# Performance work log

Hardware: AMD Instinct MI355X
Metric: run time of the kernel (lower is better)

## Reference

```python
import jax, jax.numpy as jnp
import numpy as np

B, C, H, W = 16, 384, 128, 128
RED = 6                      # reduction
CH = C // RED                # 64
CF = C // 2 + 1              # 193 rfft bins


def setup_inputs() -> dict:
    key = jax.random.key(0)
    ks = jax.random.split(key, 9)
    sc = 0.05
    return {
        "x":   jax.random.normal(ks[0], (B, C, H, W), dtype=jnp.float32),
        "W1":  jax.random.normal(ks[1], (CH, C, 3, 3), dtype=jnp.float32) * sc,
        "b1":  jax.random.normal(ks[2], (CH,), dtype=jnp.float32) * sc,
        "W2":  jax.random.normal(ks[3], (C, CH, 3, 3), dtype=jnp.float32) * sc,
        "b2":  jax.random.normal(ks[4], (C,), dtype=jnp.float32) * sc,
        "Ws1": jax.random.normal(ks[5], (CF, C), dtype=jnp.float32) * sc,
        "bs1": jax.random.normal(ks[6], (CF,), dtype=jnp.float32) * sc,
        "Ws2": jax.random.normal(ks[7], (CF, C), dtype=jnp.float32) * sc,
        "bs2": jax.random.normal(ks[8], (CF,), dtype=jnp.float32) * sc,
    }


def reference(x, W1, b1, W2, b2, Ws1, bs1, Ws2, bs2):
    b, c = x.shape[0], x.shape[1]
    # global average pool -> [b, c]
    y0 = jnp.mean(x, axis=(2, 3))
    # fc: 3x3 convs on 1x1 spatial input (pad=1) reduce to center-tap matmuls
    h = jax.nn.relu(y0 @ W1[:, :, 1, 1].T + b1)            # [b, c//red]
    y = jax.nn.sigmoid(h @ W2[:, :, 1, 1].T + b2)          # [b, c]
    # seq1 / seq2: 1x1 convs on [b, c, 1, 1]
    s1 = jax.nn.relu(y @ Ws1.T + bs1)                      # [b, c//2+1]
    s2 = jax.nn.relu(y @ Ws2.T + bs2)                      # [b, c//2+1]
    # rfft2 over (1, c) spatial dims == 1-D rfft over channel axis
    yf = jnp.fft.rfft(y, axis=-1)                          # [b, c//2+1] complex
    amp = jnp.abs(yf) * s1
    pha = jnp.angle(yf) * s2
    rec = jax.lax.complex(amp * jnp.cos(pha), amp * jnp.sin(pha))
    xr = jnp.fft.irfft(rec, n=c, axis=-1)                  # [b, c]
    out = (xr * y)[:, :, None, None]                       # [b, c, 1, 1]
    return out
```

## Files before the change

kernel.cpp:

```cpp
#include <hip/hip_runtime.h>

#define BB 16
#define CC 384
#define CH 64
#define CF 193
#define HW 16384

#define TWO_PI_OVER_CC (6.283185307179586f / (float)CC)

__global__ __launch_bounds__(256) void pool_kernel(const float4* __restrict__ x,
                                                   float* __restrict__ y0T) {
    const int c = blockIdx.x, b = blockIdx.y;
    const float4* p = x + (size_t)(b * CC + c) * (HW / 4);
    const int t = threadIdx.x;

    float s = 0.f;
#pragma unroll
    for (int r = 0; r < HW / 4 / 256; ++r) {
        float4 v = p[t + 256 * r];
        s += v.x + v.y + v.z + v.w;
    }
#pragma unroll
    for (int off = 32; off > 0; off >>= 1) s += __shfl_down(s, off);

    __shared__ float red[4];
    const int wid = t >> 6, lane = t & 63;
    if (lane == 0) red[wid] = s;
    __syncthreads();
    if (t == 0) {
        float tot = red[0] + red[1] + red[2] + red[3];
        y0T[c * BB + b] = tot * (1.0f / (float)HW);
    }
}

__global__ __launch_bounds__(256) void fc1_kernel(const float* __restrict__ y0T,
                                                  const float* __restrict__ W1,
                                                  const float* __restrict__ b1,
                                                  float* __restrict__ hT) {
    const int t = threadIdx.x;
    const int b = t & 15;
    const int j = blockIdx.x * 16 + (t >> 4);
    const float* w = W1 + (size_t)j * CC * 9 + 4;
    float acc = b1[j];
#pragma unroll 4
    for (int c = 0; c < CC; ++c) acc += y0T[c * BB + b] * w[c * 9];
    hT[j * BB + b] = fmaxf(acc, 0.f);
}

__global__ __launch_bounds__(256) void fc2_kernel(const float* __restrict__ hT,
                                                  const float* __restrict__ W2,
                                                  const float* __restrict__ b2,
                                                  float* __restrict__ yT) {
    const int t = threadIdx.x;
    const int b = t & 15;
    const int c = blockIdx.x * 16 + (t >> 4);
    const float* w = W2 + (size_t)c * CH * 9 + 4;
    float acc = b2[c];
#pragma unroll 4
    for (int j = 0; j < CH; ++j) acc += hT[j * BB + b] * w[j * 9];
    yT[c * BB + b] = 1.f / (1.f + expf(-acc));
}

__global__ __launch_bounds__(256) void spec_kernel(const float* __restrict__ yT,
                                                   const float* __restrict__ Ws1,
                                                   const float* __restrict__ bs1,
                                                   const float* __restrict__ Ws2,
                                                   const float* __restrict__ bs2,
                                                   float* __restrict__ rr,
                                                   float* __restrict__ ri) {
    __shared__ float ct[CC], st[CC];
    const int t = threadIdx.x;
    for (int i = t; i < CC; i += 256) {
        float sv, cv; sincosf((float)i * TWO_PI_OVER_CC, &sv, &cv);
        ct[i] = cv; st[i] = sv;
    }
    __syncthreads();

    const int b = t & 15;
    const int k = blockIdx.x * 16 + (t >> 4);
    if (k >= CF) return;

    const float* w1 = Ws1 + (size_t)k * CC;
    const float* w2 = Ws2 + (size_t)k * CC;
    float a1 = bs1[k], a2 = bs2[k];
    float re = 0.f, im = 0.f;
    int m = 0;
#pragma unroll 4
    for (int c = 0; c < CC; ++c) {
        float yc = yT[c * BB + b];
        a1 += yc * w1[c];
        a2 += yc * w2[c];
        re += yc * ct[m];
        im -= yc * st[m];
        m += k; if (m >= CC) m -= CC;
    }
    a1 = fmaxf(a1, 0.f);
    a2 = fmaxf(a2, 0.f);
    float amp = sqrtf(re * re + im * im) * a1;
    float pha = atan2f(im, re) * a2;
    float sp, cp; sincosf(pha, &sp, &cp);
    rr[k * BB + b] = amp * cp;
    ri[k * BB + b] = amp * sp;
}

__global__ __launch_bounds__(256) void irfft_kernel(const float* __restrict__ yT,
                                                    const float* __restrict__ rr,
                                                    const float* __restrict__ ri,
                                                    float* __restrict__ out) {
    __shared__ float ct[CC], st[CC];
    const int t = threadIdx.x;
    for (int i = t; i < CC; i += 256) {
        float sv, cv; sincosf((float)i * TWO_PI_OVER_CC, &sv, &cv);
        ct[i] = cv; st[i] = sv;
    }
    __syncthreads();

    const int c = blockIdx.x * 16 + (t & 15);
    const int b = t >> 4;

    float acc = 0.f;
    int m = 0;
#pragma unroll 4
    for (int k = 1; k < 192; ++k) {
        m += c; if (m >= CC) m -= CC;
        acc += rr[k * BB + b] * ct[m] - ri[k * BB + b] * st[m];
    }
    float nyq = (c & 1) ? -rr[192 * BB + b] : rr[192 * BB + b];
    float xr = (rr[b] + 2.f * acc + nyq) * (1.0f / (float)CC);
    out[b * CC + c] = xr * yT[c * BB + b];
}

extern "C" void kernel_launch(void* const* d_in, const int* in_sizes, int n_in,
                              void* d_out, int out_size, void* d_ws, size_t ws_size,
                              hipStream_t stream) {
    const float4* x  = (const float4*)d_in[0];
    const float* W1  = (const float*)d_in[1];
    const float* b1  = (const float*)d_in[2];
    const float* W2  = (const float*)d_in[3];
    const float* b2  = (const float*)d_in[4];
    const float* Ws1 = (const float*)d_in[5];
    const float* bs1 = (const float*)d_in[6];
    const float* Ws2 = (const float*)d_in[7];
    const float* bs2 = (const float*)d_in[8];
    float* out = (float*)d_out;

    float* ws  = (float*)d_ws;
    float* y0T = ws;
    float* hT  = y0T + CC * BB;
    float* yT  = hT  + CH * BB;
    float* rr  = yT  + CC * BB;
    float* ri  = rr  + CF * BB;

    pool_kernel <<<dim3(CC, BB), 256, 0, stream>>>(x, y0T);
    fc1_kernel  <<<CH / 16,      256, 0, stream>>>(y0T, W1, b1, hT);
    fc2_kernel  <<<CC / 16,      256, 0, stream>>>(hT, W2, b2, yT);
    spec_kernel <<<(CF + 15)/16, 256, 0, stream>>>(yT, Ws1, bs1, Ws2, bs2, rr, ri);
    irfft_kernel<<<CC / 16,      256, 0, stream>>>(yT, rr, ri, out);
}
```

Before: 645.7 us.

## Fuse fc1, fc2 and spectral stages into one redundant-compute head kernel

Merges the fc1, fc2 and spectral kernels into one head kernel. Each of its 13 blocks recomputes the full fc1 and fc2 MLP in shared memory, and then runs its own slice of the spectral stage. This drops two kernel launches and their global round trips. In exchange, the small MLP work is done 13 times over and each block runs it serially: 4 and 24 rows per thread, long dependent loops over strided weight reads. The shared-memory footprint is about 56 KB per block.

```diff
diff --git a/kernel.cpp b/kernel.cpp
--- a/kernel.cpp
+++ b/kernel.cpp
@@ -33,46 +33,48 @@
     }
 }
 
-__global__ __launch_bounds__(256) void fc1_kernel(const float* __restrict__ y0T,
-                                                  const float* __restrict__ W1,
-                                                  const float* __restrict__ b1,
-                                                  float* __restrict__ hT) {
+__global__ __launch_bounds__(256) void head_kernel(
+    const float* __restrict__ y0T,
+    const float* __restrict__ W1,  const float* __restrict__ b1,
+    const float* __restrict__ W2,  const float* __restrict__ b2,
+    const float* __restrict__ Ws1, const float* __restrict__ bs1,
+    const float* __restrict__ Ws2, const float* __restrict__ bs2,
+    float* __restrict__ yT, float* __restrict__ rr, float* __restrict__ ri)
+{
+    __shared__ float y0s[CC * BB];
+    __shared__ float hs[CH * BB];
+    __shared__ float ys[CC * BB];
+    __shared__ float ct[CC], st[CC];
+
     const int t = threadIdx.x;
-    const int b = t & 15;
-    const int j = blockIdx.x * 16 + (t >> 4);
-    const float* w = W1 + (size_t)j * CC * 9 + 4;
-    float acc = b1[j];
-#pragma unroll 4
-    for (int c = 0; c < CC; ++c) acc += y0T[c * BB + b] * w[c * 9];
-    hT[j * BB + b] = fmaxf(acc, 0.f);
-}
 
-__global__ __launch_bounds__(256) void fc2_kernel(const float* __restrict__ hT,
-                                                  const float* __restrict__ W2,
-                                                  const float* __restrict__ b2,
-                                                  float* __restrict__ yT) {
-    const int t = threadIdx.x;
-    const int b = t & 15;
-    const int c = blockIdx.x * 16 + (t >> 4);
-    const float* w = W2 + (size_t)c * CH * 9 + 4;
-    float acc = b2[c];
-#pragma unroll 4
-    for (int j = 0; j < CH; ++j) acc += hT[j * BB + b] * w[j * 9];
-    yT[c * BB + b] = 1.f / (1.f + expf(-acc));
-}
-
-__global__ __launch_bounds__(256) void spec_kernel(const float* __restrict__ yT,
-                                                   const float* __restrict__ Ws1,
-                                                   const float* __restrict__ bs1,
-                                                   const float* __restrict__ Ws2,
-                                                   const float* __restrict__ bs2,
-                                                   float* __restrict__ rr,
-                                                   float* __restrict__ ri) {
-    __shared__ float ct[CC], st[CC];
-    const int t = threadIdx.x;
     for (int i = t; i < CC; i += 256) {
         float sv, cv; sincosf((float)i * TWO_PI_OVER_CC, &sv, &cv);
         ct[i] = cv; st[i] = sv;
+    }
+    for (int i = t; i < CC * BB; i += 256) y0s[i] = y0T[i];
+    __syncthreads();
+
+#pragma unroll
+    for (int r = 0; r < 4; ++r) {
+        const int idx = t + 256 * r;
+        const int b = idx & 15, j = idx >> 4;
+        const float* w = W1 + (size_t)j * CC * 9 + 4;
+        float acc = b1[j];
+        for (int c = 0; c < CC; ++c) acc += y0s[c * BB + b] * w[c * 9];
+        hs[idx] = fmaxf(acc, 0.f);
+    }
+    __syncthreads();
+
+#pragma unroll
+    for (int r = 0; r < 24; ++r) {
+        const int idx = t + 256 * r;
+        const int b = idx & 15, c = idx >> 4;
+        const float* w = W2 + (size_t)c * CH * 9 + 4;
+        float acc = b2[c];
+        for (int j = 0; j < CH; ++j) acc += hs[j * BB + b] * w[j * 9];
+        ys[idx] = 1.f / (1.f + expf(-acc));
+        if (blockIdx.x == 0) yT[idx] = ys[idx];
     }
     __syncthreads();
 
@@ -87,7 +89,7 @@
     int m = 0;
 #pragma unroll 4
     for (int c = 0; c < CC; ++c) {
-        float yc = yT[c * BB + b];
+        float yc = ys[c * BB + b];
         a1 += yc * w1[c];
         a2 += yc * w2[c];
         re += yc * ct[m];
@@ -146,14 +148,12 @@
 
     float* ws  = (float*)d_ws;
     float* y0T = ws;
-    float* hT  = y0T + CC * BB;
-    float* yT  = hT  + CH * BB;
+    float* yT  = y0T + CC * BB;
     float* rr  = yT  + CC * BB;
     float* ri  = rr  + CF * BB;
 
     pool_kernel <<<dim3(CC, BB), 256, 0, stream>>>(x, y0T);
-    fc1_kernel  <<<CH / 16,      256, 0, stream>>>(y0T, W1, b1, hT);
-    fc2_kernel  <<<CC / 16,      256, 0, stream>>>(hT, W2, b2, yT);
-    spec_kernel <<<(CF + 15)/16, 256, 0, stream>>>(yT, Ws1, bs1, Ws2, bs2, rr, ri);
+    head_kernel <<<(CF + 15)/16, 256, 0, stream>>>(y0T, W1, b1, W2, b2,
+                                                   Ws1, bs1, Ws2, bs2, yT, rr, ri);
     irfft_kernel<<<CC / 16,      256, 0, stream>>>(yT, rr, ri, out);
 }
```

Result: no change. 653.7 us (+1.2%).
